# Performance work log

Hardware: AMD Instinct MI355X
Metric: run time of the kernel (lower is better)

## Reference

```python
import jax, jax.numpy as jnp
import numpy as np
from jax import lax

B, C, H, W = 4, 3, 512, 512
PATCH = 64
STRIDE = 32
CHANS = [(3, 32), (32, 32), (32, 64), (64, 64), (64, 64), (64, 32), (32, 32), (32, 2)]


def _conv(x, w, b):
    y = lax.conv_general_dilated(x, w, (1, 1), [(1, 1), (1, 1)],
                                 dimension_numbers=('NCHW', 'OIHW', 'NCHW'))
    return y + b[None, :, None, None]


def _pool(x):  # MaxPool2d(2)
    return lax.reduce_window(x, -jnp.inf, lax.max, (1, 1, 2, 2), (1, 1, 2, 2), 'VALID')


def _up(x):  # Upsample(scale=2, bilinear, align_corners=False) == half-pixel resize
    b, c, h, w = x.shape
    return jax.image.resize(x, (b, c, 2 * h, 2 * w), 'bilinear')


def _flow_net(x, ws, bs):
    r = jax.nn.relu
    h = r(_conv(x, ws[0], bs[0]))
    h = r(_conv(h, ws[1], bs[1]))
    h = _pool(h)
    h = r(_conv(h, ws[2], bs[2]))
    h = r(_conv(h, ws[3], bs[3]))
    h = _pool(h)
    h = _up(h)
    h = r(_conv(h, ws[4], bs[4]))
    h = r(_conv(h, ws[5], bs[5]))
    h = _up(h)
    h = r(_conv(h, ws[6], bs[6]))
    return jnp.tanh(_conv(h, ws[7], bs[7]))  # [B,2,H,W]


def _bilinear_zeros(img, gx, gy):
    # img [C,H,W], gx/gy [N,P,P] in [-1,1]; grid_sample bilinear, zeros padding, align_corners=False
    Hh, Ww = img.shape[1], img.shape[2]
    ix = ((gx + 1.0) * Ww - 1.0) * 0.5
    iy = ((gy + 1.0) * Hh - 1.0) * 0.5
    x0 = jnp.floor(ix)
    y0 = jnp.floor(iy)
    wx1 = ix - x0
    wy1 = iy - y0

    def corner(xi, yi, wgt):
        valid = (xi >= 0) & (xi <= Ww - 1) & (yi >= 0) & (yi <= Hh - 1)
        xc = jnp.clip(xi, 0, Ww - 1).astype(jnp.int32)
        yc = jnp.clip(yi, 0, Hh - 1).astype(jnp.int32)
        return img[:, yc, xc] * (wgt * valid)[None]  # [C,N,P,P]

    return (corner(x0, y0, (1 - wx1) * (1 - wy1))
            + corner(x0 + 1, y0, wx1 * (1 - wy1))
            + corner(x0, y0 + 1, (1 - wx1) * wy1)
            + corner(x0 + 1, y0 + 1, wx1 * wy1))


def _forward(x, ws, bs, temp):
    b, c, h, w = x.shape
    flow = _flow_net(x, ws, bs)  # [B,2,H,W]
    gy, gx = jnp.meshgrid(jnp.linspace(-1.0, 1.0, h), jnp.linspace(-1.0, 1.0, w), indexing='ij')
    base = jnp.stack([gx, gy], axis=-1)  # [H,W,2] (x,y)
    deformed = base[None] + flow.transpose(0, 2, 3, 1) * temp  # [B,H,W,2]
    centers = deformed[:, ::STRIDE, ::STRIDE, :].reshape(b, -1, 2)  # [B,N,2]
    py, px = jnp.meshgrid(jnp.linspace(-1.0, 1.0, PATCH), jnp.linspace(-1.0, 1.0, PATCH), indexing='ij')
    pgx = centers[:, :, None, None, 0] + px[None, None] * (PATCH / w)  # [B,N,P,P]
    pgy = centers[:, :, None, None, 1] + py[None, None] * (PATCH / h)
    patches = jax.vmap(_bilinear_zeros)(x, pgx, pgy)  # [B,C,N,P,P]
    patches = patches.transpose(0, 2, 1, 3, 4)  # [B,N,C,P,P]
    return patches, flow, deformed


def setup_inputs() -> dict:
    key = jax.random.key(0)
    ks = jax.random.split(key, len(CHANS) + 1)
    d = {"x": jax.random.normal(ks[0], (B, C, H, W), jnp.float32)}
    for i, (ci, co) in enumerate(CHANS):
        d[f"w{i}"] = jax.random.normal(ks[i + 1], (co, ci, 3, 3), jnp.float32) * 0.01
        d[f"b{i}"] = jnp.zeros((co,), jnp.float32)
    d["temp"] = jnp.full((1,), 0.1, jnp.float32)
    return d


def reference(x, w0, b0, w1, b1, w2, b2, w3, b3, w4, b4, w5, b5, w6, b6, w7, b7, temp):
    ws = [w0, w1, w2, w3, w4, w5, w6, w7]
    bs = [b0, b1, b2, b3, b4, b5, b6, b7]
    return _forward(x, ws, bs, temp)
```

## Files before the change

kernel.cpp:

```cpp
#include <hip/hip_runtime.h>
#include <hip/hip_bf16.h>

typedef __hip_bfloat16 bf16;
typedef unsigned short ushort_t;
typedef __attribute__((ext_vector_type(8))) short short8;
typedef __attribute__((ext_vector_type(4))) float float4v;

#define BATCH 4
#define HH 512
#define WW 512

__device__ __forceinline__ ushort_t f2bfu(float f) {
  __hip_bfloat16 h = __float2bfloat16(f);
  union { __hip_bfloat16 h; ushort_t u; } c;
  c.h = h;
  return c.u;
}
__device__ __forceinline__ float bfu2f(ushort_t u) {
  return __uint_as_float(((unsigned)u) << 16);
}

__device__ __forceinline__ void dma16(void* lds, const void* g) {
  __builtin_amdgcn_global_load_lds(
      (const __attribute__((address_space(1))) unsigned int*)g,
      (__attribute__((address_space(3))) unsigned int*)lds, 16, 0, 0);
}

struct WP { const float* w[8]; };

__global__ __launch_bounds__(256) void prep_w(WP wp, bf16* __restrict__ dst) {
  const int O[8]   = {32, 32, 64, 64, 64, 32, 32, 2};
  const int I[8]   = {3, 32, 32, 64, 64, 64, 32, 32};
  const int OP[8]  = {32, 32, 64, 64, 64, 32, 32, 16};
  const int IP[8]  = {32, 32, 32, 64, 64, 64, 32, 32};
  const int OFF[8] = {0, 9216, 18432, 36864, 73728, 110592, 129024, 138240};
  int l = blockIdx.y;
  int e = blockIdx.x * 256 + threadIdx.x;
  int n = 9 * OP[l] * IP[l];
  if (e >= n) return;
  int tap = e / (OP[l] * IP[l]);
  int rem = e - tap * OP[l] * IP[l];
  int o = rem / IP[l];
  int i = rem - o * IP[l];
  float v = 0.0f;
  if (o < O[l] && i < I[l]) v = wp.w[l][((o * I[l]) + i) * 9 + tap];
  dst[OFF[l] + e] = __float2bfloat16(v);
}

__global__ __launch_bounds__(256) void pack_x(const float* __restrict__ x,
                                              bf16* __restrict__ xp) {
  int i = blockIdx.x * 256 + threadIdx.x;
  if (i >= BATCH * HH * WW) return;
  int b = i / (HH * WW);
  int px = i - b * (HH * WW);
  union { uint4 v; ushort_t s[8]; } o;
  o.v = make_uint4(0, 0, 0, 0);
  const float* p = x + (long)b * 3 * HH * WW + px;
  o.s[0] = f2bfu(p[0]);
  o.s[1] = f2bfu(p[HH * WW]);
  o.s[2] = f2bfu(p[2 * HH * WW]);
  *(uint4*)&xp[(long)i * 8] = o.v;
}

template <int CIN, int COUT, int COUTR, int ACT, int IN_MODE, int OUT_MODE>
__global__ __launch_bounds__(256) void conv_mfma(
    const void* __restrict__ in_, const bf16* __restrict__ wt,
    const float* __restrict__ bias, void* __restrict__ out_, int H, int W,
    const float* __restrict__ temp, float* __restrict__ def) {
  constexpr int MT = COUT / 16;
  constexpr int CK = 32;
  __shared__ alignas(16) bf16 in_lds[324 * CK];
  __shared__ alignas(16) bf16 w_lds[9 * COUT * CK];

  const int tid = threadIdx.x;
  const int lane = tid & 63;
  const int wid = tid >> 6;
  const int lm = lane & 15;
  const int quad = lane >> 4;
  const int x0 = blockIdx.x * 16;
  const int y0 = blockIdx.y * 16;
  const int b = blockIdx.z;

  float4v acc[MT][4];
#pragma unroll
  for (int mt = 0; mt < MT; ++mt) {
    float4v bv;
    if constexpr (COUTR == COUT) {
      bv = *(const float4v*)(bias + mt * 16 + quad * 4);
    } else {
#pragma unroll
      for (int r = 0; r < 4; ++r) {
        int co = mt * 16 + quad * 4 + r;
        bv[r] = (co < COUTR) ? bias[co] : 0.0f;
      }
    }
#pragma unroll
    for (int nt = 0; nt < 4; ++nt) acc[mt][nt] = bv;
  }

  for (int c0 = 0; c0 < CIN; c0 += CK) {
    if constexpr (IN_MODE == 3) {
      const bf16* in = (const bf16*)in_;
      for (int u = tid; u < 324 * 4; u += 256) {
        int px = u >> 2;
        int seg = u & 3;
        int hy = px / 18, hx = px - hy * 18;
        int gy = y0 - 1 + hy, gx = x0 - 1 + hx;
        uint4 v = make_uint4(0, 0, 0, 0);
        if (seg == 0 && gy >= 0 && gy < H && gx >= 0 && gx < W)
          v = *(const uint4*)(in + (((long)b * H + gy) * W + gx) * 8);
        *(uint4*)&in_lds[px * CK + seg * 8] = v;
      }
    } else if constexpr (IN_MODE == 2) {
      const bf16* in = (const bf16*)in_;
      const int Hs = H >> 1, Ws = W >> 1;
      for (int u = tid; u < 324 * 4; u += 256) {
        int px = u >> 2;
        int seg = u & 3;
        int hy = px / 18, hx = px - hy * 18;
        int gy = y0 - 1 + hy, gx = x0 - 1 + hx;
        uint4 o = make_uint4(0, 0, 0, 0);
        if (gy >= 0 && gy < H && gx >= 0 && gx < W) {
          int ys = (gy >> 1) - ((gy & 1) ? 0 : 1);
          int xs = (gx >> 1) - ((gx & 1) ? 0 : 1);
          float wy = (gy & 1) ? 0.25f : 0.75f;
          float wx = (gx & 1) ? 0.25f : 0.75f;
          int y0c = max(ys, 0), y1c = min(ys + 1, Hs - 1);
          int x0c = max(xs, 0), x1c = min(xs + 1, Ws - 1);
          const bf16* p = in + ((long)b * Hs * Ws) * CIN + c0 + seg * 8;
          union { uint4 v; ushort_t s[8]; } a00, a01, a10, a11, r;
          a00.v = *(const uint4*)(p + ((long)y0c * Ws + x0c) * CIN);
          a01.v = *(const uint4*)(p + ((long)y0c * Ws + x1c) * CIN);
          a10.v = *(const uint4*)(p + ((long)y1c * Ws + x0c) * CIN);
          a11.v = *(const uint4*)(p + ((long)y1c * Ws + x1c) * CIN);
#pragma unroll
          for (int j = 0; j < 8; ++j) {
            float f = (1.0f - wy) * ((1.0f - wx) * bfu2f(a00.s[j]) +
                                     wx * bfu2f(a01.s[j])) +
                      wy * ((1.0f - wx) * bfu2f(a10.s[j]) +
                            wx * bfu2f(a11.s[j]));
            r.s[j] = f2bfu(f);
          }
          o = r.v;
        }
        *(uint4*)&in_lds[px * CK + seg * 8] = o;
      }
    } else {
      const bool interior =
          (x0 >= 1) && (x0 + 16 <= W - 1) && (y0 >= 1) && (y0 + 16 <= H - 1);
      const bf16* in = (const bf16*)in_;
      if (interior) {
        for (int r = wid; r < 18; r += 4) {
          int gy = y0 - 1 + r;
          const bf16* gsrc = in + (((long)b * H + gy) * W + x0) * CIN + c0 +
                             (lane >> 2) * CIN + (lane & 3) * 8;
          dma16(&in_lds[(r * 18 + 1) * CK], gsrc);
        }
        if (tid < 144) {
          int r = tid >> 3;
          int side = (tid >> 2) & 1;
          int seg = tid & 3;
          int gx = side ? (x0 + 16) : (x0 - 1);
          int gy = y0 - 1 + r;
          uint4 v = *(const uint4*)(in + (((long)b * H + gy) * W + gx) * CIN +
                                    c0 + seg * 8);
          *(uint4*)&in_lds[(r * 18 + (side ? 17 : 0)) * CK + seg * 8] = v;
        }
      } else {
        for (int u = tid; u < 324 * 4; u += 256) {
          int px = u >> 2;
          int seg = u & 3;
          int hy = px / 18, hx = px - hy * 18;
          int gy = y0 - 1 + hy, gx = x0 - 1 + hx;
          uint4 v = make_uint4(0, 0, 0, 0);
          if (gy >= 0 && gy < H && gx >= 0 && gx < W)
            v = *(const uint4*)(in + (((long)b * H + gy) * W + gx) * CIN + c0 +
                                seg * 8);
          *(uint4*)&in_lds[px * CK + seg * 8] = v;
        }
      }
    }
    {
      constexpr int WUNITS = 9 * COUT * CK / 8;
      for (int u = tid; u < WUNITS; u += 256) {
        int to = u >> 2;
        int seg = u & 3;
        uint4 v = *(const uint4*)(wt + (long)to * CIN + c0 + seg * 8);
        *(uint4*)&w_lds[to * CK + seg * 8] = v;
      }
    }
    __syncthreads();

#pragma unroll
    for (int tap = 0; tap < 9; ++tap) {
      const int r = tap / 3, s = tap - r * 3;
      short8 afrag[MT], bfrag[4];
#pragma unroll
      for (int mt = 0; mt < MT; ++mt)
        afrag[mt] =
            *(const short8*)&w_lds[(tap * COUT + mt * 16 + lm) * CK + quad * 8];
#pragma unroll
      for (int nt = 0; nt < 4; ++nt) {
        int py = 4 * wid + nt;
        bfrag[nt] =
            *(const short8*)&in_lds[((py + r) * 18 + lm + s) * CK + quad * 8];
      }
#pragma unroll
      for (int mt = 0; mt < MT; ++mt)
#pragma unroll
        for (int nt = 0; nt < 4; ++nt)
          acc[mt][nt] = __builtin_amdgcn_mfma_f32_16x16x32_bf16(
              afrag[mt], bfrag[nt], acc[mt][nt], 0, 0, 0);
    }
    __syncthreads();
  }

  if constexpr (OUT_MODE == 3) {
    bf16* out = (bf16*)out_;
    const int Ho = H >> 1, Wo = W >> 1;
#pragma unroll
    for (int mt = 0; mt < MT; ++mt) {
#pragma unroll
      for (int g = 0; g < 2; ++g) {
        float4v m;
#pragma unroll
        for (int r = 0; r < 4; ++r)
          m[r] = fmaxf(fmaxf(acc[mt][2 * g][r], acc[mt][2 * g + 1][r]), 0.0f);
#pragma unroll
        for (int r = 0; r < 4; ++r) m[r] = fmaxf(m[r], __shfl_xor(m[r], 1, 64));
        if ((lm & 1) == 0) {
          int pyo = (y0 >> 1) + 2 * wid + g;
          int pxo = (x0 >> 1) + (lm >> 1);
          union { uint2 v; ushort_t s[4]; } pk;
#pragma unroll
          for (int r = 0; r < 4; ++r) pk.s[r] = f2bfu(m[r]);
          *(uint2*)&out[(((long)b * Ho + pyo) * Wo + pxo) * COUT + mt * 16 +
                        quad * 4] = pk.v;
        }
      }
    }
  } else {
#pragma unroll
    for (int mt = 0; mt < MT; ++mt) {
#pragma unroll
      for (int nt = 0; nt < 4; ++nt) {
        int gy = y0 + 4 * wid + nt;
        int gx = x0 + lm;
        float4v v = acc[mt][nt];
        if constexpr (OUT_MODE == 0) {
          bf16* out = (bf16*)out_;
          union { uint2 v; ushort_t s[4]; } pk;
#pragma unroll
          for (int r = 0; r < 4; ++r) pk.s[r] = f2bfu(fmaxf(v[r], 0.0f));
          *(uint2*)&out[(((long)b * H + gy) * W + gx) * COUT + mt * 16 +
                        quad * 4] = pk.v;
        } else {
          float* out = (float*)out_;
          if (quad == 0) {
            float fx = tanhf(v[0]);
            float fy = tanhf(v[1]);
            out[(((long)b * 2 + 0) * H + gy) * (long)W + gx] = fx;
            out[(((long)b * 2 + 1) * H + gy) * (long)W + gx] = fy;
            float T = temp[0];
            float2 d;
            d.x = -1.0f + gx * (2.0f / 511.0f) + fx * T;
            d.y = -1.0f + gy * (2.0f / 511.0f) + fy * T;
            *(float2*)&def[(((long)b * H + gy) * W + gx) * 2] = d;
          }
        }
      }
    }
  }
}

__global__ __launch_bounds__(256) void patches_k(const float* __restrict__ x,
                                                 const float* __restrict__ def,
                                                 float* __restrict__ out) {
  int i = blockIdx.x * 256 + threadIdx.x;
  int pj = i & 63;
  int t = i >> 6;
  int pi = t & 63;
  t >>= 6;
  int n = t & 255;
  int b = t >> 8;
  if (b >= BATCH) return;
  int hi = n >> 4, wi = n & 15;
  const float* dptr = def + (((long)b * HH + hi * 32) * WW + wi * 32) * 2;
  float cx = dptr[0], cy = dptr[1];
  float pgx = cx + (-1.0f + pj * (2.0f / 63.0f)) * 0.125f;
  float pgy = cy + (-1.0f + pi * (2.0f / 63.0f)) * 0.125f;
  float ix = ((pgx + 1.0f) * 512.0f - 1.0f) * 0.5f;
  float iy = ((pgy + 1.0f) * 512.0f - 1.0f) * 0.5f;
  float fx0 = floorf(ix), fy0 = floorf(iy);
  float wx1 = ix - fx0, wy1 = iy - fy0;
  int x0 = (int)fx0, y0 = (int)fy0;
  int x1 = x0 + 1, y1 = y0 + 1;
  bool vx0 = (x0 >= 0) && (x0 <= 511), vx1 = (x1 >= 0) && (x1 <= 511);
  bool vy0 = (y0 >= 0) && (y0 <= 511), vy1 = (y1 >= 0) && (y1 <= 511);
  int cx0 = min(max(x0, 0), 511), cx1 = min(max(x1, 0), 511);
  int cy0 = min(max(y0, 0), 511), cy1 = min(max(y1, 0), 511);
  float w00 = (1.0f - wx1) * (1.0f - wy1) * ((vx0 && vy0) ? 1.0f : 0.0f);
  float w01 = wx1 * (1.0f - wy1) * ((vx1 && vy0) ? 1.0f : 0.0f);
  float w10 = (1.0f - wx1) * wy1 * ((vx0 && vy1) ? 1.0f : 0.0f);
  float w11 = wx1 * wy1 * ((vx1 && vy1) ? 1.0f : 0.0f);
#pragma unroll
  for (int c = 0; c < 3; ++c) {
    const float* img = x + ((long)b * 3 + c) * (HH * WW);
    float v = img[cy0 * WW + cx0] * w00 + img[cy0 * WW + cx1] * w01 +
              img[cy1 * WW + cx0] * w10 + img[cy1 * WW + cx1] * w11;
    out[(((long)b * 256 + n) * 3 + c) * 4096 + pi * 64 + pj] = v;
  }
}


extern "C" void kernel_launch(void* const* d_in, const int* in_sizes, int n_in,
                              void* d_out, int out_size, void* d_ws,
                              size_t ws_size, hipStream_t stream) {
  const float* x = (const float*)d_in[0];
  WP wp;
  const float* bs[8];
  for (int i = 0; i < 8; ++i) {
    wp.w[i] = (const float*)d_in[1 + 2 * i];
    bs[i] = (const float*)d_in[2 + 2 * i];
  }
  const float* temp = (const float*)d_in[17];

  float* out = (float*)d_out;
  float* flow = out + 12582912;
  float* def = out + 14680064;

  bf16* wT = (bf16*)d_out;
  const int WOFF[8] = {0, 9216, 18432, 36864, 73728, 110592, 129024, 138240};

  const size_t bufElems = (size_t)BATCH * 512 * 512 * 32;
  bf16* A = (bf16*)d_ws;
  bf16* Bf = A + bufElems;
  bf16* xp = Bf + bufElems;

  prep_w<<<dim3(144, 8), 256, 0, stream>>>(wp, wT);
  {
    int total = BATCH * HH * WW;
    pack_x<<<(total + 255) / 256, 256, 0, stream>>>(x, xp);
  }

  dim3 g512(32, 32, BATCH);
  dim3 g256(16, 16, BATCH);
  dim3 g128(8, 8, BATCH);

  conv_mfma<32, 32, 32, 0, 3, 0>
      <<<g512, 256, 0, stream>>>(xp, wT + WOFF[0], bs[0], A, 512, 512, nullptr, nullptr);
  conv_mfma<32, 32, 32, 0, 0, 3>
      <<<g512, 256, 0, stream>>>(A, wT + WOFF[1], bs[1], Bf, 512, 512, nullptr, nullptr);
  conv_mfma<32, 64, 64, 0, 0, 0>
      <<<g256, 256, 0, stream>>>(Bf, wT + WOFF[2], bs[2], A, 256, 256, nullptr, nullptr);
  conv_mfma<64, 64, 64, 0, 0, 3>
      <<<g256, 256, 0, stream>>>(A, wT + WOFF[3], bs[3], Bf, 256, 256, nullptr, nullptr);
  conv_mfma<64, 64, 64, 0, 2, 0>
      <<<g256, 256, 0, stream>>>(Bf, wT + WOFF[4], bs[4], A, 256, 256, nullptr, nullptr);
  conv_mfma<64, 32, 32, 0, 0, 0>
      <<<g256, 256, 0, stream>>>(A, wT + WOFF[5], bs[5], Bf, 256, 256, nullptr, nullptr);
  conv_mfma<32, 32, 32, 0, 2, 0>
      <<<g512, 256, 0, stream>>>(Bf, wT + WOFF[6], bs[6], A, 512, 512, nullptr, nullptr);
  conv_mfma<32, 16, 2, 1, 0, 2>
      <<<g512, 256, 0, stream>>>(A, wT + WOFF[7], bs[7], flow, 512, 512, temp, def);
  {
    int total = BATCH * 256 * 64 * 64;
    patches_k<<<(total + 255) / 256, 256, 0, stream>>>(x, def, out);
  }
}
```

Measured before the change: 354.3 us.

## Fold bilinear upsample into polyphase conv weights, pack first-layer taps, DMA weights

The 2x bilinear upsample followed by a 3x3 conv is rewritten as four polyphase 3x3 convolutions on the low-resolution map. Their weights are precomputed in prep_w, and a separate ring_fix kernel computes the border pixels where clamping breaks the polyphase identity. The first layer gets a dedicated kernel that packs taps over its 3 real input channels instead of padding them to 32. Weight tiles are now loaded into LDS with global_load_lds DMA. Together these remove the upsample interpolation work and the zero-padded MFMA work, at the cost of more kernels and extra border-correctness logic.

```diff
diff --git a/kernel.cpp b/kernel.cpp
--- a/kernel.cpp
+++ b/kernel.cpp
@@ -9,6 +9,15 @@
 #define BATCH 4
 #define HH 512
 #define WW 512
+
+#define WO_L0 0
+#define WO_L1 3072
+#define WO_L2 12288
+#define WO_L3 30720
+#define WO_L4P 67584
+#define WO_L5 215040
+#define WO_L6P 233472
+#define WO_L7 270336
 
 __device__ __forceinline__ ushort_t f2bfu(float f) {
   __hip_bfloat16 h = __float2bfloat16(f);
@@ -16,9 +25,6 @@
   c.h = h;
   return c.u;
 }
-__device__ __forceinline__ float bfu2f(ushort_t u) {
-  return __uint_as_float(((unsigned)u) << 16);
-}
 
 __device__ __forceinline__ void dma16(void* lds, const void* g) {
   __builtin_amdgcn_global_load_lds(
@@ -26,25 +32,74 @@
       (__attribute__((address_space(3))) unsigned int*)lds, 16, 0, 0);
 }
 
+__device__ __forceinline__ float upw(int k, int u) {
+  int lo = k >> 1;
+  float a = (k & 1) ? 0.25f : 0.75f;
+  float b = (k & 1) ? 0.75f : 0.25f;
+  return (u == lo) ? a : (u == lo + 1) ? b : 0.0f;
+}
+
 struct WP { const float* w[8]; };
 
 __global__ __launch_bounds__(256) void prep_w(WP wp, bf16* __restrict__ dst) {
-  const int O[8]   = {32, 32, 64, 64, 64, 32, 32, 2};
-  const int I[8]   = {3, 32, 32, 64, 64, 64, 32, 32};
-  const int OP[8]  = {32, 32, 64, 64, 64, 32, 32, 16};
-  const int IP[8]  = {32, 32, 32, 64, 64, 64, 32, 32};
-  const int OFF[8] = {0, 9216, 18432, 36864, 73728, 110592, 129024, 138240};
-  int l = blockIdx.y;
-  int e = blockIdx.x * 256 + threadIdx.x;
-  int n = 9 * OP[l] * IP[l];
+  const int job = blockIdx.y;
+  const int e = blockIdx.x * 256 + threadIdx.x;
+  if (job == 0) {
+    if (e >= 3072) return;
+    int c = e & 7;
+    int o = (e >> 3) & 31;
+    int g = (e >> 8) % 3;
+    int tl = (e >> 8) / 3;
+    int tap = g * 4 + tl;
+    float v = 0.0f;
+    if (tap < 9 && c < 3) v = wp.w[0][(o * 3 + c) * 9 + tap];
+    dst[WO_L0 + e] = __float2bfloat16(v);
+    return;
+  }
+  if (job == 4 || job == 6) {
+    const int O = (job == 4) ? 64 : 32;
+    const int I = O;
+    const int NCH = I >> 5;
+    const int n = 4 * NCH * 9 * O * 32;
+    if (e >= n) return;
+    int ic = e & 31;
+    int o = (e >> 5) % O;
+    int tap = (e / (32 * O)) % 9;
+    int ch = (e / (9 * 32 * O)) % NCH;
+    int ph = e / (NCH * 9 * 32 * O);
+    int i = ch * 32 + ic;
+    int u = tap / 3, v2 = tap - u * 3;
+    int dy = ph >> 1, dx = ph & 1;
+    const float* w = wp.w[job];
+    float acc = 0.0f;
+#pragma unroll
+    for (int r = 0; r < 3; ++r) {
+      float ry = upw(r + dy, u);
+#pragma unroll
+      for (int s = 0; s < 3; ++s)
+        acc += w[(o * I + i) * 9 + r * 3 + s] * ry * upw(s + dx, v2);
+    }
+    dst[((job == 4) ? WO_L4P : WO_L6P) + e] = __float2bfloat16(acc);
+    return;
+  }
+  int O, I, OP, off;
+  const float* w;
+  if (job == 1)      { O = 32; I = 32; OP = 32; off = WO_L1; w = wp.w[1]; }
+  else if (job == 2) { O = 64; I = 32; OP = 64; off = WO_L2; w = wp.w[2]; }
+  else if (job == 3) { O = 64; I = 64; OP = 64; off = WO_L3; w = wp.w[3]; }
+  else if (job == 5) { O = 32; I = 64; OP = 32; off = WO_L5; w = wp.w[5]; }
+  else               { O = 2;  I = 32; OP = 16; off = WO_L7; w = wp.w[7]; }
+  const int NCH = I >> 5;
+  const int n = NCH * 9 * OP * 32;
   if (e >= n) return;
-  int tap = e / (OP[l] * IP[l]);
-  int rem = e - tap * OP[l] * IP[l];
-  int o = rem / IP[l];
-  int i = rem - o * IP[l];
+  int ic = e & 31;
+  int o = (e >> 5) % OP;
+  int tap = (e / (32 * OP)) % 9;
+  int ch = e / (9 * 32 * OP);
+  int i = ch * 32 + ic;
   float v = 0.0f;
-  if (o < O[l] && i < I[l]) v = wp.w[l][((o * I[l]) + i) * 9 + tap];
-  dst[OFF[l] + e] = __float2bfloat16(v);
+  if (o < O) v = w[(o * I + i) * 9 + tap];
+  dst[off + e] = __float2bfloat16(v);
 }
 
 __global__ __launch_bounds__(256) void pack_x(const float* __restrict__ x,
@@ -62,16 +117,90 @@
   *(uint4*)&xp[(long)i * 8] = o.v;
 }
 
-template <int CIN, int COUT, int COUTR, int ACT, int IN_MODE, int OUT_MODE>
+__global__ __launch_bounds__(256) void conv0_k(
+    const bf16* __restrict__ xp, const bf16* __restrict__ wt,
+    const float* __restrict__ bias, bf16* __restrict__ out) {
+  __shared__ alignas(16) bf16 in_lds[324 * 8];
+  __shared__ alignas(16) bf16 w_lds[3072];
+  const int tid = threadIdx.x;
+  const int lane = tid & 63;
+  const int wid = tid >> 6;
+  const int lm = lane & 15;
+  const int quad = lane >> 4;
+  const int x0 = blockIdx.x * 16, y0 = blockIdx.y * 16;
+  const int b = blockIdx.z;
+
+#pragma unroll
+  for (int k = 0; k < 2; ++k) {
+    int u = tid + k * 256;
+    if (u < 324) {
+      int hy = u / 18, hx = u - hy * 18;
+      int gy = y0 - 1 + hy, gx = x0 - 1 + hx;
+      uint4 v = make_uint4(0, 0, 0, 0);
+      if (gy >= 0 && gy < HH && gx >= 0 && gx < WW)
+        v = *(const uint4*)(xp + (((long)b * HH + gy) * WW + gx) * 8);
+      *(uint4*)&in_lds[u * 8] = v;
+    }
+  }
+#pragma unroll
+  for (int k = 0; k < 2; ++k) {
+    int u = tid + k * 256;
+    if (u < 384) *(uint4*)&w_lds[u * 8] = *(const uint4*)(wt + u * 8);
+  }
+  __syncthreads();
+
+  float4v acc[2][4];
+#pragma unroll
+  for (int mt = 0; mt < 2; ++mt) {
+    float4v bv = *(const float4v*)(bias + mt * 16 + quad * 4);
+#pragma unroll
+    for (int nt = 0; nt < 4; ++nt) acc[mt][nt] = bv;
+  }
+
+#pragma unroll
+  for (int g = 0; g < 3; ++g) {
+    int tap = g * 4 + quad;
+    if (tap > 8) tap = 8;
+    int r = (tap * 11) >> 5;
+    int s = tap - r * 3;
+    short8 afrag[2], bfrag[4];
+#pragma unroll
+    for (int mt = 0; mt < 2; ++mt)
+      afrag[mt] = *(const short8*)&w_lds[quad * 768 + (g * 32 + mt * 16 + lm) * 8];
+#pragma unroll
+    for (int nt = 0; nt < 4; ++nt) {
+      int py = 4 * wid + nt;
+      bfrag[nt] = *(const short8*)&in_lds[((py + r) * 18 + lm + s) * 8];
+    }
+#pragma unroll
+    for (int mt = 0; mt < 2; ++mt)
+#pragma unroll
+      for (int nt = 0; nt < 4; ++nt)
+        acc[mt][nt] = __builtin_amdgcn_mfma_f32_16x16x32_bf16(
+            afrag[mt], bfrag[nt], acc[mt][nt], 0, 0, 0);
+  }
+
+#pragma unroll
+  for (int mt = 0; mt < 2; ++mt)
+#pragma unroll
+    for (int nt = 0; nt < 4; ++nt) {
+      int gy = y0 + 4 * wid + nt, gx = x0 + lm;
+      union { uint2 v; ushort_t s2[4]; } pk;
+#pragma unroll
+      for (int r2 = 0; r2 < 4; ++r2) pk.s2[r2] = f2bfu(fmaxf(acc[mt][nt][r2], 0.0f));
+      *(uint2*)&out[(((long)b * HH + gy) * WW + gx) * 32 + mt * 16 + quad * 4] = pk.v;
+    }
+}
+
+template <int CIN, int COUT, int COUTR, int OUT_MODE>
 __global__ __launch_bounds__(256) void conv_mfma(
-    const void* __restrict__ in_, const bf16* __restrict__ wt,
+    const bf16* __restrict__ in, const bf16* __restrict__ wt,
     const float* __restrict__ bias, void* __restrict__ out_, int H, int W,
     const float* __restrict__ temp, float* __restrict__ def) {
   constexpr int MT = COUT / 16;
   constexpr int CK = 32;
   __shared__ alignas(16) bf16 in_lds[324 * CK];
   __shared__ alignas(16) bf16 w_lds[9 * COUT * CK];
-
   const int tid = threadIdx.x;
   const int lane = tid & 63;
   const int wid = tid >> 6;
@@ -98,96 +227,44 @@
     for (int nt = 0; nt < 4; ++nt) acc[mt][nt] = bv;
   }
 
+  const bool interior =
+      (x0 >= 1) && (x0 + 16 <= W - 1) && (y0 >= 1) && (y0 + 16 <= H - 1);
   for (int c0 = 0; c0 < CIN; c0 += CK) {
-    if constexpr (IN_MODE == 3) {
-      const bf16* in = (const bf16*)in_;
+    if (interior) {
+      for (int r = wid; r < 18; r += 4) {
+        int gy = y0 - 1 + r;
+        const bf16* gsrc = in + (((long)b * H + gy) * W + x0) * CIN + c0 +
+                           (lane >> 2) * CIN + (lane & 3) * 8;
+        dma16(&in_lds[(r * 18 + 1) * CK], gsrc);
+      }
+      if (tid < 144) {
+        int r = tid >> 3;
+        int side = (tid >> 2) & 1;
+        int seg = tid & 3;
+        int gx = side ? (x0 + 16) : (x0 - 1);
+        int gy = y0 - 1 + r;
+        uint4 v = *(const uint4*)(in + (((long)b * H + gy) * W + gx) * CIN +
+                                  c0 + seg * 8);
+        *(uint4*)&in_lds[(r * 18 + (side ? 17 : 0)) * CK + seg * 8] = v;
+      }
+    } else {
       for (int u = tid; u < 324 * 4; u += 256) {
         int px = u >> 2;
         int seg = u & 3;
         int hy = px / 18, hx = px - hy * 18;
         int gy = y0 - 1 + hy, gx = x0 - 1 + hx;
         uint4 v = make_uint4(0, 0, 0, 0);
-        if (seg == 0 && gy >= 0 && gy < H && gx >= 0 && gx < W)
-          v = *(const uint4*)(in + (((long)b * H + gy) * W + gx) * 8);
+        if (gy >= 0 && gy < H && gx >= 0 && gx < W)
+          v = *(const uint4*)(in + (((long)b * H + gy) * W + gx) * CIN + c0 +
+                              seg * 8);
         *(uint4*)&in_lds[px * CK + seg * 8] = v;
       }
-    } else if constexpr (IN_MODE == 2) {
-      const bf16* in = (const bf16*)in_;
-      const int Hs = H >> 1, Ws = W >> 1;
-      for (int u = tid; u < 324 * 4; u += 256) {
-        int px = u >> 2;
-        int seg = u & 3;
-        int hy = px / 18, hx = px - hy * 18;
-        int gy = y0 - 1 + hy, gx = x0 - 1 + hx;
-        uint4 o = make_uint4(0, 0, 0, 0);
-        if (gy >= 0 && gy < H && gx >= 0 && gx < W) {
-          int ys = (gy >> 1) - ((gy & 1) ? 0 : 1);
-          int xs = (gx >> 1) - ((gx & 1) ? 0 : 1);
-          float wy = (gy & 1) ? 0.25f : 0.75f;
-          float wx = (gx & 1) ? 0.25f : 0.75f;
-          int y0c = max(ys, 0), y1c = min(ys + 1, Hs - 1);
-          int x0c = max(xs, 0), x1c = min(xs + 1, Ws - 1);
-          const bf16* p = in + ((long)b * Hs * Ws) * CIN + c0 + seg * 8;
-          union { uint4 v; ushort_t s[8]; } a00, a01, a10, a11, r;
-          a00.v = *(const uint4*)(p + ((long)y0c * Ws + x0c) * CIN);
-          a01.v = *(const uint4*)(p + ((long)y0c * Ws + x1c) * CIN);
-          a10.v = *(const uint4*)(p + ((long)y1c * Ws + x0c) * CIN);
-          a11.v = *(const uint4*)(p + ((long)y1c * Ws + x1c) * CIN);
-#pragma unroll
-          for (int j = 0; j < 8; ++j) {
-            float f = (1.0f - wy) * ((1.0f - wx) * bfu2f(a00.s[j]) +
-                                     wx * bfu2f(a01.s[j])) +
-                      wy * ((1.0f - wx) * bfu2f(a10.s[j]) +
-                            wx * bfu2f(a11.s[j]));
-            r.s[j] = f2bfu(f);
-          }
-          o = r.v;
-        }
-        *(uint4*)&in_lds[px * CK + seg * 8] = o;
-      }
-    } else {
-      const bool interior =
-          (x0 >= 1) && (x0 + 16 <= W - 1) && (y0 >= 1) && (y0 + 16 <= H - 1);
-      const bf16* in = (const bf16*)in_;
-      if (interior) {
-        for (int r = wid; r < 18; r += 4) {
-          int gy = y0 - 1 + r;
-          const bf16* gsrc = in + (((long)b * H + gy) * W + x0) * CIN + c0 +
-                             (lane >> 2) * CIN + (lane & 3) * 8;
-          dma16(&in_lds[(r * 18 + 1) * CK], gsrc);
-        }
-        if (tid < 144) {
-          int r = tid >> 3;
-          int side = (tid >> 2) & 1;
-          int seg = tid & 3;
-          int gx = side ? (x0 + 16) : (x0 - 1);
-          int gy = y0 - 1 + r;
-          uint4 v = *(const uint4*)(in + (((long)b * H + gy) * W + gx) * CIN +
-                                    c0 + seg * 8);
-          *(uint4*)&in_lds[(r * 18 + (side ? 17 : 0)) * CK + seg * 8] = v;
-        }
-      } else {
-        for (int u = tid; u < 324 * 4; u += 256) {
-          int px = u >> 2;
-          int seg = u & 3;
-          int hy = px / 18, hx = px - hy * 18;
-          int gy = y0 - 1 + hy, gx = x0 - 1 + hx;
-          uint4 v = make_uint4(0, 0, 0, 0);
-          if (gy >= 0 && gy < H && gx >= 0 && gx < W)
-            v = *(const uint4*)(in + (((long)b * H + gy) * W + gx) * CIN + c0 +
-                                seg * 8);
-          *(uint4*)&in_lds[px * CK + seg * 8] = v;
-        }
-      }
     }
     {
-      constexpr int WUNITS = 9 * COUT * CK / 8;
-      for (int u = tid; u < WUNITS; u += 256) {
-        int to = u >> 2;
-        int seg = u & 3;
-        uint4 v = *(const uint4*)(wt + (long)to * CIN + c0 + seg * 8);
-        *(uint4*)&w_lds[to * CK + seg * 8] = v;
-      }
+      const char* wsrc = (const char*)(wt + (size_t)(c0 >> 5) * 9 * COUT * CK);
+      constexpr int WCH = 9 * COUT * CK * 2 / 1024;
+      for (int j = wid; j < WCH; j += 4)
+        dma16((char*)w_lds + j * 1024, wsrc + j * 1024 + lane * 16);
     }
     __syncthreads();
 
@@ -265,12 +342,174 @@
             float2 d;
             d.x = -1.0f + gx * (2.0f / 511.0f) + fx * T;
             d.y = -1.0f + gy * (2.0f / 511.0f) + fy * T;
-            *(float2*)&def[(((long)b * H + gy) * W + gx) * 2] = d;
+            *(float2*)&def[(((long)b * HH + gy) * WW + gx) * 2] = d;
           }
         }
       }
     }
   }
+}
+
+template <int CIN, int COUT>
+__global__ __launch_bounds__(256) void conv_up(
+    const bf16* __restrict__ in, const bf16* __restrict__ wt,
+    const float* __restrict__ bias, bf16* __restrict__ out, int Ho, int Wo) {
+  constexpr int MT = COUT / 16;
+  constexpr int CK = 32;
+  __shared__ alignas(16) bf16 in_lds[324 * CK];
+  __shared__ alignas(16) bf16 w_lds[9 * COUT * CK];
+  const int tid = threadIdx.x;
+  const int lane = tid & 63;
+  const int wid = tid >> 6;
+  const int lm = lane & 15;
+  const int quad = lane >> 4;
+  const int Hs = Ho >> 1, Ws = Wo >> 1;
+  const int NB = Wo >> 5;
+  const int bx = blockIdx.x, by = blockIdx.y;
+  const int xs0 = bx * 16, ys0 = by * 16;
+  const int b = blockIdx.z;
+  const bool interior = (bx >= 1) && (bx < NB - 1) && (by >= 1) && (by < NB - 1);
+
+  for (int ph = 0; ph < 4; ++ph) {
+    float4v acc[MT][4];
+#pragma unroll
+    for (int mt = 0; mt < MT; ++mt) {
+      float4v bv = *(const float4v*)(bias + mt * 16 + quad * 4);
+#pragma unroll
+      for (int nt = 0; nt < 4; ++nt) acc[mt][nt] = bv;
+    }
+    for (int c0 = 0; c0 < CIN; c0 += CK) {
+      if (ph == 0 || CIN > CK) {
+        if (interior) {
+          for (int r = wid; r < 18; r += 4) {
+            int gy = ys0 - 1 + r;
+            const bf16* gsrc = in + (((long)b * Hs + gy) * Ws + xs0) * CIN +
+                               c0 + (lane >> 2) * CIN + (lane & 3) * 8;
+            dma16(&in_lds[(r * 18 + 1) * CK], gsrc);
+          }
+          if (tid < 144) {
+            int r = tid >> 3;
+            int side = (tid >> 2) & 1;
+            int seg = tid & 3;
+            int gx = side ? (xs0 + 16) : (xs0 - 1);
+            int gy = ys0 - 1 + r;
+            uint4 v = *(const uint4*)(in + (((long)b * Hs + gy) * Ws + gx) * CIN +
+                                      c0 + seg * 8);
+            *(uint4*)&in_lds[(r * 18 + (side ? 17 : 0)) * CK + seg * 8] = v;
+          }
+        } else {
+          for (int u = tid; u < 324 * 4; u += 256) {
+            int px = u >> 2;
+            int seg = u & 3;
+            int hy = px / 18, hx = px - hy * 18;
+            int sy = min(max(ys0 - 1 + hy, 0), Hs - 1);
+            int sx = min(max(xs0 - 1 + hx, 0), Ws - 1);
+            uint4 v = *(const uint4*)(in + (((long)b * Hs + sy) * Ws + sx) * CIN +
+                                      c0 + seg * 8);
+            *(uint4*)&in_lds[px * CK + seg * 8] = v;
+          }
+        }
+      }
+      {
+        const char* wsrc = (const char*)(wt + (size_t)(ph * (CIN / CK) + (c0 >> 5)) *
+                                                  9 * COUT * CK);
+        constexpr int WCH = 9 * COUT * CK * 2 / 1024;
+        for (int j = wid; j < WCH; j += 4)
+          dma16((char*)w_lds + j * 1024, wsrc + j * 1024 + lane * 16);
+      }
+      __syncthreads();
+#pragma unroll
+      for (int tap = 0; tap < 9; ++tap) {
+        const int r = tap / 3, s = tap - r * 3;
+        short8 afrag[MT], bfrag[4];
+#pragma unroll
+        for (int mt = 0; mt < MT; ++mt)
+          afrag[mt] =
+              *(const short8*)&w_lds[(tap * COUT + mt * 16 + lm) * CK + quad * 8];
+#pragma unroll
+        for (int nt = 0; nt < 4; ++nt) {
+          int py = 4 * wid + nt;
+          bfrag[nt] =
+              *(const short8*)&in_lds[((py + r) * 18 + lm + s) * CK + quad * 8];
+        }
+#pragma unroll
+        for (int mt = 0; mt < MT; ++mt)
+#pragma unroll
+          for (int nt = 0; nt < 4; ++nt)
+            acc[mt][nt] = __builtin_amdgcn_mfma_f32_16x16x32_bf16(
+                afrag[mt], bfrag[nt], acc[mt][nt], 0, 0, 0);
+      }
+      __syncthreads();
+    }
+    const int dy = ph >> 1, dx = ph & 1;
+#pragma unroll
+    for (int mt = 0; mt < MT; ++mt)
+#pragma unroll
+      for (int nt = 0; nt < 4; ++nt) {
+        int gy = 2 * (ys0 + 4 * wid + nt) + dy;
+        int gx = 2 * (xs0 + lm) + dx;
+        union { uint2 v; ushort_t s2[4]; } pk;
+#pragma unroll
+        for (int r2 = 0; r2 < 4; ++r2)
+          pk.s2[r2] = f2bfu(fmaxf(acc[mt][nt][r2], 0.0f));
+        *(uint2*)&out[(((long)b * Ho + gy) * Wo + gx) * COUT + mt * 16 +
+                      quad * 4] = pk.v;
+      }
+  }
+}
+
+template <int CIN, int COUT>
+__global__ __launch_bounds__(256) void ring_fix(
+    const bf16* __restrict__ src, const float* __restrict__ wf,
+    const float* __restrict__ bias, bf16* __restrict__ out, int Ho, int Wo) {
+  constexpr int OG = COUT / 8;
+  int i = blockIdx.x * 256 + threadIdx.x;
+  int ring = 2 * Wo + 2 * (Ho - 2);
+  int total = BATCH * ring * OG;
+  if (i >= total) return;
+  int og = i % OG;
+  int pxi = i / OG;
+  int b = pxi / ring;
+  int t = pxi - b * ring;
+  int gy, gx;
+  if (t < Wo) { gy = 0; gx = t; }
+  else if (t < 2 * Wo) { gy = Ho - 1; gx = t - Wo; }
+  else { int u = t - 2 * Wo; gy = 1 + (u >> 1); gx = (u & 1) ? (Wo - 1) : 0; }
+  int Hs = Ho >> 1, Ws = Wo >> 1;
+  float acc[8];
+#pragma unroll
+  for (int j = 0; j < 8; ++j) acc[j] = bias[og * 8 + j];
+  for (int r = 0; r < 3; ++r)
+    for (int s = 0; s < 3; ++s) {
+      int uy = gy - 1 + r, ux = gx - 1 + s;
+      if (uy < 0 || uy >= Ho || ux < 0 || ux >= Wo) continue;
+      int ys = (uy >> 1) - ((uy & 1) ? 0 : 1);
+      int xs = (ux >> 1) - ((ux & 1) ? 0 : 1);
+      float wy = (uy & 1) ? 0.25f : 0.75f;
+      float wx = (ux & 1) ? 0.25f : 0.75f;
+      int y0c = max(ys, 0), y1c = min(ys + 1, Hs - 1);
+      int x0c = max(xs, 0), x1c = min(xs + 1, Ws - 1);
+      const bf16* p00 = src + (((long)b * Hs + y0c) * Ws + x0c) * CIN;
+      const bf16* p01 = src + (((long)b * Hs + y0c) * Ws + x1c) * CIN;
+      const bf16* p10 = src + (((long)b * Hs + y1c) * Ws + x0c) * CIN;
+      const bf16* p11 = src + (((long)b * Hs + y1c) * Ws + x1c) * CIN;
+      const float* wtap = wf + r * 3 + s;
+#pragma unroll 8
+      for (int ci = 0; ci < CIN; ++ci) {
+        float up =
+            (1.0f - wy) * ((1.0f - wx) * __bfloat162float(p00[ci]) +
+                           wx * __bfloat162float(p01[ci])) +
+            wy * ((1.0f - wx) * __bfloat162float(p10[ci]) +
+                  wx * __bfloat162float(p11[ci]));
+#pragma unroll
+        for (int j = 0; j < 8; ++j)
+          acc[j] += wtap[(((og * 8 + j) * CIN) + ci) * 9] * up;
+      }
+    }
+  union { uint4 v; ushort_t us[8]; } pk;
+#pragma unroll
+  for (int j = 0; j < 8; ++j) pk.us[j] = f2bfu(fmaxf(acc[j], 0.0f));
+  *(uint4*)&out[(((long)b * Ho + gy) * Wo + gx) * COUT + og * 8] = pk.v;
 }
 
 __global__ __launch_bounds__(256) void patches_k(const float* __restrict__ x,
@@ -328,43 +567,33 @@
   float* out = (float*)d_out;
   float* flow = out + 12582912;
   float* def = out + 14680064;
-
   bf16* wT = (bf16*)d_out;
-  const int WOFF[8] = {0, 9216, 18432, 36864, 73728, 110592, 129024, 138240};
 
   const size_t bufElems = (size_t)BATCH * 512 * 512 * 32;
   bf16* A = (bf16*)d_ws;
   bf16* Bf = A + bufElems;
   bf16* xp = Bf + bufElems;
 
-  prep_w<<<dim3(144, 8), 256, 0, stream>>>(wp, wT);
-  {
-    int total = BATCH * HH * WW;
-    pack_x<<<(total + 255) / 256, 256, 0, stream>>>(x, xp);
-  }
+  prep_w<<<dim3(576, 8), 256, 0, stream>>>(wp, wT);
+  pack_x<<<(BATCH * HH * WW) / 256, 256, 0, stream>>>(x, xp);
 
   dim3 g512(32, 32, BATCH);
   dim3 g256(16, 16, BATCH);
-  dim3 g128(8, 8, BATCH);
-
-  conv_mfma<32, 32, 32, 0, 3, 0>
-      <<<g512, 256, 0, stream>>>(xp, wT + WOFF[0], bs[0], A, 512, 512, nullptr, nullptr);
-  conv_mfma<32, 32, 32, 0, 0, 3>
-      <<<g512, 256, 0, stream>>>(A, wT + WOFF[1], bs[1], Bf, 512, 512, nullptr, nullptr);
-  conv_mfma<32, 64, 64, 0, 0, 0>
-      <<<g256, 256, 0, stream>>>(Bf, wT + WOFF[2], bs[2], A, 256, 256, nullptr, nullptr);
-  conv_mfma<64, 64, 64, 0, 0, 3>
-      <<<g256, 256, 0, stream>>>(A, wT + WOFF[3], bs[3], Bf, 256, 256, nullptr, nullptr);
-  conv_mfma<64, 64, 64, 0, 2, 0>
-      <<<g256, 256, 0, stream>>>(Bf, wT + WOFF[4], bs[4], A, 256, 256, nullptr, nullptr);
-  conv_mfma<64, 32, 32, 0, 0, 0>
-      <<<g256, 256, 0, stream>>>(A, wT + WOFF[5], bs[5], Bf, 256, 256, nullptr, nullptr);
-  conv_mfma<32, 32, 32, 0, 2, 0>
-      <<<g512, 256, 0, stream>>>(Bf, wT + WOFF[6], bs[6], A, 512, 512, nullptr, nullptr);
-  conv_mfma<32, 16, 2, 1, 0, 2>
-      <<<g512, 256, 0, stream>>>(A, wT + WOFF[7], bs[7], flow, 512, 512, temp, def);
-  {
-    int total = BATCH * 256 * 64 * 64;
-    patches_k<<<(total + 255) / 256, 256, 0, stream>>>(x, def, out);
-  }
-}
+
+  conv0_k<<<g512, 256, 0, stream>>>(xp, wT + WO_L0, bs[0], A);
+  conv_mfma<32, 32, 32, 3>
+      <<<g512, 256, 0, stream>>>(A, wT + WO_L1, bs[1], Bf, 512, 512, nullptr, nullptr);
+  conv_mfma<32, 64, 64, 0>
+      <<<g256, 256, 0, stream>>>(Bf, wT + WO_L2, bs[2], A, 256, 256, nullptr, nullptr);
+  conv_mfma<64, 64, 64, 3>
+      <<<g256, 256, 0, stream>>>(A, wT + WO_L3, bs[3], Bf, 256, 256, nullptr, nullptr);
+  conv_up<64, 64><<<dim3(8, 8, BATCH), 256, 0, stream>>>(Bf, wT + WO_L4P, bs[4], A, 256, 256);
+  ring_fix<64, 64><<<128, 256, 0, stream>>>(Bf, wp.w[4], bs[4], A, 256, 256);
+  conv_mfma<64, 32, 32, 0>
+      <<<g256, 256, 0, stream>>>(A, wT + WO_L5, bs[5], Bf, 256, 256, nullptr, nullptr);
+  conv_up<32, 32><<<dim3(16, 16, BATCH), 256, 0, stream>>>(Bf, wT + WO_L6P, bs[6], A, 512, 512);
+  ring_fix<32, 32><<<128, 256, 0, stream>>>(Bf, wp.w[6], bs[6], A, 512, 512);
+  conv_mfma<32, 16, 2, 2>
+      <<<g512, 256, 0, stream>>>(A, wT + WO_L7, bs[7], flow, 512, 512, temp, def);
+  patches_k<<<(BATCH * 256 * 64 * 64) / 256, 256, 0, stream>>>(x, def, out);
+}
```

Result: slower. 661.0 us (+86.6%).
